# Performance work log

Measured on AMD Instinct MI355X. Metric: run time of the kernel, lower is better.

Reference implementation:

```python
import jax, jax.numpy as jnp
import numpy as np

N, E, D, S, H, L = 20000, 320000, 128, 16, 4, 64


def _ln(x, g, b):
    m = x.mean(-1, keepdims=True)
    v = jnp.mean((x - m) ** 2, -1, keepdims=True)
    return (x - m) / jnp.sqrt(v + 1e-6) * g + b


def _mlp3(x, w1, b1, g1, be1, w2, b2, g2, be2, w3, b3):
    h = jax.nn.silu(_ln(x @ w1 + b1, g1, be1))
    h = jax.nn.silu(_ln(h @ w2 + b2, g2, be2))
    return h @ w3 + b3


def _seg_softmax(a, idx, n):
    # torch_geometric.utils.softmax: per-destination-group stable softmax
    m = jax.ops.segment_max(a, idx, num_segments=n)
    m = jnp.where(jnp.isfinite(m), m, 0.0)
    e = jnp.exp(a - m[idx])
    s = jax.ops.segment_sum(e, idx, num_segments=n)
    return e / (s[idx] + 1e-16)


def setup_inputs() -> dict:
    key = jax.random.key(0)
    ks = jax.random.split(key, 32)
    rn = lambda k, sh, sc=1.0: jax.random.normal(k, sh, dtype=jnp.float32) * sc
    li = lambda k, fi, fo: rn(k, (fi, fo), 1.0 / np.sqrt(fi))
    z = lambda n_: jnp.zeros((n_,), jnp.float32)
    o = lambda n_: jnp.ones((n_,), jnp.float32)
    inp = {
        'node_in': rn(ks[0], (N, D)),
        'node_embed': rn(ks[1], (N, D)),
        'edge_sh': rn(ks[2], (E, S)),
        'edge_length_embedding': rn(ks[3], (E, L)),
        'edge_src': jax.random.randint(ks[4], (E,), 0, N, dtype=jnp.int32),
        'edge_dst': jax.random.randint(ks[5], (E,), 0, N, dtype=jnp.int32),
        'batch': jnp.zeros((N,), jnp.int32),
        'pre_lin_w': li(ks[6], 2 * D + L, D),
        'tp2_w1': li(ks[7], L, 64), 'tp2_b1': z(64),
        'tp2_w2': li(ks[8], 64, H * S), 'tp2_b2': z(H * S),
        'a_w1': li(ks[9], L, 64), 'a_b1': z(64), 'a_g1': o(64), 'a_be1': z(64),
        'a_w2': li(ks[10], 64, 64), 'a_b2': z(64), 'a_g2': o(64), 'a_be2': z(64),
        'a_w3': li(ks[11], 64, H), 'a_b3': z(H),
        'lin_w': li(ks[12], D * H, D),
        'lin_edge_w': li(ks[13], D * H, 64),
        's_w1': li(ks[14], 64, 64), 's_b1': z(64), 's_g1': o(64), 's_be1': z(64),
        's_w2': li(ks[15], 64, 64), 's_b2': z(64), 's_g2': o(64), 's_be2': z(64),
        's_w3': li(ks[16], 64, 32), 's_b3': z(32),
    }
    return inp


def reference(node_in, node_embed, edge_sh, edge_length_embedding, edge_src, edge_dst, batch,
              pre_lin_w, tp2_w1, tp2_b1, tp2_w2, tp2_b2,
              a_w1, a_b1, a_g1, a_be1, a_w2, a_b2, a_g2, a_be2, a_w3, a_b3,
              lin_w, lin_edge_w,
              s_w1, s_b1, s_g1, s_be1, s_w2, s_b2, s_g2, s_be2, s_w3, s_b3):
    e = edge_length_embedding.shape[0]
    n = node_in.shape[0]
    # gather + pre_lin
    msg = jnp.concatenate([node_in[edge_src], node_in[edge_dst], edge_length_embedding], -1) @ pre_lin_w  # [E,D]
    # EquiConv tp2: channelwise TP with radial-MLP per-edge per-(head,sh) weights
    radial = jax.nn.silu(edge_length_embedding @ tp2_w1 + tp2_b1) @ tp2_w2 + tp2_b2  # [E,H*S]
    scal = jnp.einsum('ehs,es->eh', radial.reshape(e, H, S), edge_sh)  # [E,H]
    value = msg[:, None, :] * scal[:, :, None]  # [E,H,D]
    alpha = _mlp3(edge_length_embedding, a_w1, a_b1, a_g1, a_be1, a_w2, a_b2, a_g2, a_be2, a_w3, a_b3)  # [E,H]
    edge_out = value * alpha[:, :, None]  # [E,H,D]
    edge_scalar = _mlp3(edge_out.reshape(e, -1) @ lin_edge_w,
                        s_w1, s_b1, s_g1, s_be1, s_w2, s_b2, s_g2, s_be2, s_w3, s_b3)  # [E,32]
    asm = _seg_softmax(alpha, edge_dst, n)  # [E,H]
    node_fea = jax.ops.segment_sum(value * asm[:, :, None], edge_dst, num_segments=n)  # [N,H,D]
    node_out = node_fea.reshape(n, -1) @ lin_w  # [N,D]
    return node_out, edge_scalar
```

## Files before the change

kernel.cpp:

```cpp
#include <hip/hip_runtime.h>

#define NN 20000
#define EE 320000
#define WTOT 27648
#define P3N (EE*64/8 + NN*128/8)

typedef unsigned short u16;
typedef unsigned int u32;
typedef __attribute__((ext_vector_type(8))) short bf16x8;
typedef __attribute__((ext_vector_type(8))) _Float16 f16x8;
typedef __attribute__((ext_vector_type(4))) float f32x4;

__device__ __forceinline__ float bf2f(u16 u){
  union { u32 i; float f; } v; v.i = ((u32)u) << 16; return v.f;
}
__device__ __forceinline__ u16 f2bf(float f){
  union { float f; u32 i; } v; v.f = f;
  u32 i = v.i;
  return (u16)((i + 0x7FFFu + ((i >> 16) & 1u)) >> 16);
}
__device__ __forceinline__ u16 f2h(float f){
  union { _Float16 h[2]; u32 u; } v; v.h[0] = (_Float16)f;
  return (u16)(v.u & 0xFFFF);
}
__device__ __forceinline__ float h2f(u16 u){
  union { u32 i; _Float16 h[2]; } v; v.i = u; return (float)v.h[0];
}
__device__ __forceinline__ u32 packh2(float a, float b){
  return ((u32)f2h(b) << 16) | (u32)f2h(a);
}
__device__ __forceinline__ float fsilu(float y){
  return y * __builtin_amdgcn_rcpf(1.f + __expf(-y));
}

__global__ __launch_bounds__(256) void k_prep_all(
    const float* __restrict__ elen, const float* __restrict__ node_in,
    u16* __restrict__ elen16, u16* __restrict__ node16,
    int* __restrict__ counts,
    const float* __restrict__ plw, const float* __restrict__ lew,
    const float* __restrict__ lw,
    u16* __restrict__ Bt1, u16* __restrict__ Bt2, u16* __restrict__ Bt3,
    const float* __restrict__ aw1, const float* __restrict__ aw2, const float* __restrict__ aw3,
    const float* __restrict__ rw1, const float* __restrict__ rw2,
    const float* __restrict__ sw1, const float* __restrict__ sw2, const float* __restrict__ sw3,
    u16* __restrict__ W)
{
  size_t gi = (size_t)blockIdx.x * 256 + threadIdx.x;
  if (gi < (size_t)P3N) {
    const size_t n1 = (size_t)EE * 64 / 8;
    const float* src;
    u16* dst;
    if (gi < n1) { src = elen + gi*8; dst = elen16 + gi*8; }
    else { size_t j = gi - n1; src = node_in + j*8; dst = node16 + j*8; }
    float4 a = ((const float4*)src)[0];
    float4 b = ((const float4*)src)[1];
    uint4 vh;
    vh.x = packh2(a.x, a.y); vh.y = packh2(a.z, a.w);
    vh.z = packh2(b.x, b.y); vh.w = packh2(b.z, b.w);
    *(uint4*)dst = vh;
    return;
  }
  long j = (long)gi - P3N;
  if (j < NN) { counts[j] = 0; return; }
  j -= NN;
  if (j < 128*320) {
    int n = (int)j / 320, k = (int)j % 320;
    Bt1[j] = f2h(plw[k*128 + n]);
    return;
  }
  j -= 128*320;
  if (j < 256*128) {
    int n = (int)j / 128, k = (int)j % 128;
    int h = n >> 6, c = n & 63;
    Bt2[j] = f2h(lew[(h*128 + k)*64 + c]);
    return;
  }
  j -= 256*128;
  if (j < 128*512) {
    int n = (int)j / 512, k = (int)j % 512;
    Bt3[j] = f2bf(lw[k*128 + n]);
    return;
  }
  j -= 128*512;
  if (j < WTOT) {
    float v = 0.f;
    long i = j;
    if (i < 8192)      { int n = i >> 6, k = i & 63;
                         v = (n < 64) ? aw1[k*64 + n] : rw1[k*64 + (n - 64)]; }
    else if ((i -= 8192) < 4096) { int n = i >> 6, k = i & 63; v = aw2[k*64 + n]; }
    else if ((i -= 4096) < 1024) { int n = i >> 6, k = i & 63; v = (n < 4) ? aw3[k*4 + n] : 0.f; }
    else if ((i -= 1024) < 4096) { int n = i >> 6, k = i & 63; v = rw2[k*64 + n]; }
    else if ((i -= 4096) < 4096) { int n = i >> 6, k = i & 63; v = sw1[k*64 + n]; }
    else if ((i -= 4096) < 4096) { int n = i >> 6, k = i & 63; v = sw2[k*64 + n]; }
    else               { i -= 4096; int n = i >> 6, k = i & 63; v = sw3[k*32 + n]; }
    W[j] = f2h(v);
  }
}

__global__ __launch_bounds__(256) void k_count(const int* __restrict__ edst, int* __restrict__ counts){
  int e = blockIdx.x * 256 + threadIdx.x;
  if (e < EE) atomicAdd(&counts[edst[e]], 1);
}
__global__ __launch_bounds__(1024) void k_scan(const int* __restrict__ counts,
                                               int* __restrict__ offs, int* __restrict__ cursor){
  __shared__ int part[1024];
  int t = threadIdx.x;
  int c0 = t * 20, c1 = c0 + 20; if (c1 > NN) c1 = NN; if (c0 > NN) c0 = NN;
  int s = 0;
  for (int i = c0; i < c1; ++i) s += counts[i];
  part[t] = s;
  __syncthreads();
  int acc = s;
  #pragma unroll
  for (int d = 1; d < 1024; d <<= 1) {
    int v = (t >= d) ? part[t - d] : 0;
    __syncthreads();
    acc += v;
    part[t] = acc;
    __syncthreads();
  }
  if (t == 1023) offs[NN] = acc;
  int run = acc - s;
  for (int i = c0; i < c1; ++i) { offs[i] = run; cursor[i] = run; run += counts[i]; }
}
__global__ __launch_bounds__(256) void k_fill(const int* __restrict__ edst,
                                              int* __restrict__ cursor, int* __restrict__ eids){
  int e = blockIdx.x * 256 + threadIdx.x;
  if (e < EE) { int p = atomicAdd(&cursor[edst[e]], 1); eids[p] = e; }
}
__global__ __launch_bounds__(256) void k_sort2(const int* __restrict__ offs, int* __restrict__ eids){
  int w = threadIdx.x >> 6, lane = threadIdx.x & 63;
  int n = blockIdx.x * 4 + w;
  if (n >= NN) return;
  int beg = offs[n], end = offs[n+1], deg = end - beg;
  if (deg <= 1) return;
  if (deg <= 64) {
    int v = (lane < deg) ? eids[beg + lane] : 0x7fffffff;
    int rank = 0;
    for (int j = 0; j < deg; ++j) {
      int u = __shfl(v, j);
      rank += (u < v) ? 1 : 0;
    }
    if (lane < deg) eids[beg + rank] = v;
  } else if (lane == 0) {
    for (int i = beg + 1; i < end; ++i) {
      int v = eids[i]; int j = i - 1;
      while (j >= beg && eids[j] > v) { eids[j+1] = eids[j]; --j; }
      eids[j+1] = v;
    }
  }
}

template<int NI>
__device__ __forceinline__ void gemm16_lds(const u16 (*X)[72], int wrow, int lane,
                                           const u16* __restrict__ B, f32x4 acc[2][4])
{
  const int fr = lane & 15, fc = lane >> 4;
  #pragma unroll
  for (int mi = 0; mi < 2; ++mi)
    #pragma unroll
    for (int ni = 0; ni < NI; ++ni)
      acc[mi][ni] = (f32x4){0.f, 0.f, 0.f, 0.f};
  #pragma unroll
  for (int kk = 0; kk < 2; ++kk) {
    f16x8 a0 = *(const f16x8*)&X[wrow + fr][kk*32 + fc*8];
    f16x8 a1 = *(const f16x8*)&X[wrow + 16 + fr][kk*32 + fc*8];
    #pragma unroll
    for (int ni = 0; ni < NI; ++ni) {
      f16x8 b = *(const f16x8*)(B + (size_t)(ni*16 + fr)*64 + kk*32 + fc*8);
      acc[0][ni] = __builtin_amdgcn_mfma_f32_16x16x32_f16(a0, b, acc[0][ni], 0, 0, 0);
      acc[1][ni] = __builtin_amdgcn_mfma_f32_16x16x32_f16(a1, b, acc[1][ni], 0, 0, 0);
    }
  }
}

template<int NI>
__device__ __forceinline__ void gemm16_lds1(const u16 (*X)[72], int wrow, int lane,
                                            const u16* __restrict__ B, f32x4 acc[4])
{
  const int fr = lane & 15, fc = lane >> 4;
  #pragma unroll
  for (int ni = 0; ni < NI; ++ni) acc[ni] = (f32x4){0.f, 0.f, 0.f, 0.f};
  #pragma unroll
  for (int kk = 0; kk < 2; ++kk) {
    f16x8 a = *(const f16x8*)&X[wrow + fr][kk*32 + fc*8];
    #pragma unroll
    for (int ni = 0; ni < NI; ++ni) {
      f16x8 b = *(const f16x8*)(B + (size_t)(ni*16 + fr)*64 + kk*32 + fc*8);
      acc[ni] = __builtin_amdgcn_mfma_f32_16x16x32_f16(a, b, acc[ni], 0, 0, 0);
    }
  }
}

__device__ __forceinline__ void gemm16_glb8(const u16* __restrict__ X, int row0, int lane,
                                            const u16* __restrict__ B, f32x4 acc[2][8])
{
  const int fr = lane & 15, fc = lane >> 4;
  #pragma unroll
  for (int mi = 0; mi < 2; ++mi)
    #pragma unroll
    for (int ni = 0; ni < 8; ++ni)
      acc[mi][ni] = (f32x4){0.f, 0.f, 0.f, 0.f};
  #pragma unroll
  for (int kk = 0; kk < 2; ++kk) {
    f16x8 a0 = *(const f16x8*)(X + (size_t)(row0 + fr)*64 + kk*32 + fc*8);
    f16x8 a1 = *(const f16x8*)(X + (size_t)(row0 + 16 + fr)*64 + kk*32 + fc*8);
    #pragma unroll
    for (int ni = 0; ni < 8; ++ni) {
      f16x8 b = *(const f16x8*)(B + (size_t)(ni*16 + fr)*64 + kk*32 + fc*8);
      acc[0][ni] = __builtin_amdgcn_mfma_f32_16x16x32_f16(a0, b, acc[0][ni], 0, 0, 0);
      acc[1][ni] = __builtin_amdgcn_mfma_f32_16x16x32_f16(a1, b, acc[1][ni], 0, 0, 0);
    }
  }
}

template<bool LN>
__device__ __forceinline__ void act_store16(f32x4 acc[2][4],
    const float* __restrict__ b, const float* __restrict__ g, const float* __restrict__ be,
    u16 (*H)[72], int wrow, int lane)
{
  const int fr = lane & 15, fc = lane >> 4;
  float bv[4], gv[4], bev[4];
  #pragma unroll
  for (int ni = 0; ni < 4; ++ni) {
    bv[ni] = b[ni*16 + fr];
    if (LN) { gv[ni] = g[ni*16 + fr]; bev[ni] = be[ni*16 + fr]; }
  }
  #pragma unroll
  for (int mi = 0; mi < 2; ++mi)
    #pragma unroll
    for (int j = 0; j < 4; ++j) {
      int r = wrow + mi*16 + fc*4 + j;
      float x[4];
      #pragma unroll
      for (int ni = 0; ni < 4; ++ni) x[ni] = acc[mi][ni][j] + bv[ni];
      if (LN) {
        float s  = x[0] + x[1] + x[2] + x[3];
        float s2 = x[0]*x[0] + x[1]*x[1] + x[2]*x[2] + x[3]*x[3];
        #pragma unroll
        for (int off = 1; off < 16; off <<= 1) {
          s  += __shfl_xor(s,  off);
          s2 += __shfl_xor(s2, off);
        }
        float mu  = s * (1.f/64.f);
        float var = s2 * (1.f/64.f) - mu*mu;
        float rs  = rsqrtf(var + 1e-6f);
        #pragma unroll
        for (int ni = 0; ni < 4; ++ni) x[ni] = (x[ni] - mu)*rs*gv[ni] + bev[ni];
      }
      #pragma unroll
      for (int ni = 0; ni < 4; ++ni)
        H[r][ni*16 + fr] = f2h(fsilu(x[ni]));
    }
}

template<bool LN>
__device__ __forceinline__ void act_store16_1(f32x4 acc[4],
    const float* __restrict__ b, const float* __restrict__ g, const float* __restrict__ be,
    u16 (*H)[72], int wrow, int lane)
{
  const int fr = lane & 15, fc = lane >> 4;
  float bv[4], gv[4], bev[4];
  #pragma unroll
  for (int ni = 0; ni < 4; ++ni) {
    bv[ni] = b[ni*16 + fr];
    if (LN) { gv[ni] = g[ni*16 + fr]; bev[ni] = be[ni*16 + fr]; }
  }
  #pragma unroll
  for (int j = 0; j < 4; ++j) {
    int r = wrow + fc*4 + j;
    float x[4];
    #pragma unroll
    for (int ni = 0; ni < 4; ++ni) x[ni] = acc[ni][j] + bv[ni];
    if (LN) {
      float s  = x[0] + x[1] + x[2] + x[3];
      float s2 = x[0]*x[0] + x[1]*x[1] + x[2]*x[2] + x[3]*x[3];
      #pragma unroll
      for (int off = 1; off < 16; off <<= 1) {
        s  += __shfl_xor(s,  off);
        s2 += __shfl_xor(s2, off);
      }
      float mu  = s * (1.f/64.f);
      float var = s2 * (1.f/64.f) - mu*mu;
      float rs  = rsqrtf(var + 1e-6f);
      #pragma unroll
      for (int ni = 0; ni < 4; ++ni) x[ni] = (x[ni] - mu)*rs*gv[ni] + bev[ni];
    }
    #pragma unroll
    for (int ni = 0; ni < 4; ++ni)
      H[r][ni*16 + fr] = f2h(fsilu(x[ni]));
  }
}

union ESmem {
  struct { u16 Ha[128][72]; u16 Hr[128][72]; } m;
  struct { u16 Bs[2][128][40]; } g;
};
__global__ __launch_bounds__(256, 4) void k_edge1(
  const u16* __restrict__ elen16, const float* __restrict__ esh,
  const u16* __restrict__ Wm,
  const float* __restrict__ ab1, const float* __restrict__ ag1, const float* __restrict__ abe1,
  const float* __restrict__ ab2, const float* __restrict__ ag2, const float* __restrict__ abe2,
  const float* __restrict__ ab3,
  const float* __restrict__ tb1, const float* __restrict__ tb2,
  float* __restrict__ alpha_g, float* __restrict__ scal_g, float* __restrict__ cbuf_g,
  const u16* __restrict__ node16,
  const int* __restrict__ esrc, const int* __restrict__ edst,
  const u16* __restrict__ Bt1, u16* __restrict__ msgb)
{
  __shared__ ESmem u;
  __shared__ float aS[128][4];
  const u16* Wc1 = Wm;
  const u16* Wa2 = Wm + 8192;
  const u16* Wa3 = Wm + 12288;
  const u16* Wr2 = Wm + 13312;
  const int tid = threadIdx.x;
  const int wave = tid >> 6, lane = tid & 63;
  const int fr = lane & 15, fc = lane >> 4;
  const int wrow = wave * 32;
  const int e0 = blockIdx.x * 128;
  {
    {
      f32x4 acc8[2][8];
      gemm16_glb8(elen16, e0 + wrow, lane, Wc1, acc8);
      float bva[4], gva[4], beva[4], bvr[4];
      #pragma unroll
      for (int ni = 0; ni < 4; ++ni) {
        bva[ni] = ab1[ni*16 + fr]; gva[ni] = ag1[ni*16 + fr]; beva[ni] = abe1[ni*16 + fr];
        bvr[ni] = tb1[ni*16 + fr];
      }
      #pragma unroll
      for (int mi = 0; mi < 2; ++mi)
        #pragma unroll
        for (int j = 0; j < 4; ++j) {
          int r = wrow + mi*16 + fc*4 + j;
          float xa[4], xr[4];
          #pragma unroll
          for (int ni = 0; ni < 4; ++ni) {
            xa[ni] = acc8[mi][ni][j] + bva[ni];
            xr[ni] = acc8[mi][ni+4][j] + bvr[ni];
          }
          float s  = xa[0] + xa[1] + xa[2] + xa[3];
          float s2 = xa[0]*xa[0] + xa[1]*xa[1] + xa[2]*xa[2] + xa[3]*xa[3];
          #pragma unroll
          for (int off = 1; off < 16; off <<= 1) {
            s  += __shfl_xor(s,  off);
            s2 += __shfl_xor(s2, off);
          }
          float mu  = s * (1.f/64.f);
          float var = s2 * (1.f/64.f) - mu*mu;
          float rs  = rsqrtf(var + 1e-6f);
          #pragma unroll
          for (int ni = 0; ni < 4; ++ni) {
            float y = (xa[ni] - mu)*rs*gva[ni] + beva[ni];
            u.m.Ha[r][ni*16 + fr] = f2h(fsilu(y));
            u.m.Hr[r][ni*16 + fr] = f2h(fsilu(xr[ni]));
          }
        }
    }
    f32x4 acc[2][4];
    gemm16_lds<4>(u.m.Ha, wrow, lane, Wa2, acc);
    act_store16<true>(acc, ab2, ag2, abe2, u.m.Ha, wrow, lane);
    gemm16_lds<1>(u.m.Ha, wrow, lane, Wa3, acc);
    {
      float bv = (fr < 4) ? ab3[fr] : 0.f;
      #pragma unroll
      for (int mi = 0; mi < 2; ++mi)
        #pragma unroll
        for (int j = 0; j < 4; ++j) {
          int r = wrow + mi*16 + fc*4 + j;
          float v = acc[mi][0][j] + bv;
          if (fr < 4) {
            alpha_g[(size_t)(e0 + r)*4 + fr] = v;
            aS[r][fr] = v;
          }
        }
    }
    gemm16_lds<4>(u.m.Hr, wrow, lane, Wr2, acc);
    {
      float bv[4];
      #pragma unroll
      for (int ni = 0; ni < 4; ++ni) bv[ni] = tb2[ni*16 + fr];
      #pragma unroll
      for (int mi = 0; mi < 2; ++mi)
        #pragma unroll
        for (int j = 0; j < 4; ++j) {
          int r = wrow + mi*16 + fc*4 + j;
          float shv = esh[(size_t)(e0 + r)*16 + fr];
          float sc[4];
          #pragma unroll
          for (int ni = 0; ni < 4; ++ni) {
            float t = (acc[mi][ni][j] + bv[ni]) * shv;
            #pragma unroll
            for (int off = 1; off < 16; off <<= 1) t += __shfl_xor(t, off);
            sc[ni] = t;
          }
          if (fr == 0) {
            float4 sv; sv.x = sc[0]; sv.y = sc[1]; sv.z = sc[2]; sv.w = sc[3];
            *(float4*)(scal_g + (size_t)(e0 + r)*4) = sv;
            float4 cv;
            cv.x = sc[0]*aS[r][0]; cv.y = sc[1]*aS[r][1];
            cv.z = sc[2]*aS[r][2]; cv.w = sc[3]*aS[r][3];
            *(float4*)(cbuf_g + (size_t)(e0 + r)*4) = cv;
          }
        }
    }
  }
  __syncthreads();
  {
    const int r0 = e0 + wrow + fr;
    const int r1 = r0 + 16;
    const int s0 = esrc[r0], d0 = edst[r0];
    const int s1 = esrc[r1], d1 = edst[r1];
    const int sr = tid >> 1, sh = tid & 1;
    const u16* bstg = Bt1 + (size_t)sr*320 + sh*16;
    {
      const uint4* bp = (const uint4*)(bstg);
      *(uint4*)&u.g.Bs[0][sr][sh*16]     = bp[0];
      *(uint4*)&u.g.Bs[0][sr][sh*16 + 8] = bp[1];
    }
    f32x4 acc[2][8];
    #pragma unroll
    for (int mi = 0; mi < 2; ++mi)
      #pragma unroll
      for (int ni = 0; ni < 8; ++ni)
        acc[mi][ni] = (f32x4){0.f, 0.f, 0.f, 0.f};
    __syncthreads();
    #pragma unroll
    for (int k0i = 0; k0i < 10; ++k0i) {
      const int buf = k0i & 1;
      if (k0i + 1 < 10) {
        const uint4* bp = (const uint4*)(bstg + (k0i + 1)*32);
        *(uint4*)&u.g.Bs[buf^1][sr][sh*16]     = bp[0];
        *(uint4*)&u.g.Bs[buf^1][sr][sh*16 + 8] = bp[1];
      }
      const int k0 = k0i * 32;
      const u16 *ap0, *ap1;
      if (k0 < 128)      { ap0 = node16 + (size_t)s0*128 + k0;
                           ap1 = node16 + (size_t)s1*128 + k0; }
      else if (k0 < 256) { ap0 = node16 + (size_t)d0*128 + (k0 - 128);
                           ap1 = node16 + (size_t)d1*128 + (k0 - 128); }
      else               { ap0 = elen16 + (size_t)r0*64 + (k0 - 256);
                           ap1 = elen16 + (size_t)r1*64 + (k0 - 256); }
      f16x8 a0 = *(const f16x8*)(ap0 + fc*8);
      f16x8 a1 = *(const f16x8*)(ap1 + fc*8);
      #pragma unroll
      for (int ni = 0; ni < 8; ++ni) {
        f16x8 b = *(const f16x8*)&u.g.Bs[buf][ni*16 + fr][fc*8];
        acc[0][ni] = __builtin_amdgcn_mfma_f32_16x16x32_f16(a0, b, acc[0][ni], 0, 0, 0);
        acc[1][ni] = __builtin_amdgcn_mfma_f32_16x16x32_f16(a1, b, acc[1][ni], 0, 0, 0);
      }
      __syncthreads();
    }
    #pragma unroll
    for (int mi = 0; mi < 2; ++mi)
      #pragma unroll
      for (int j = 0; j < 4; ++j) {
        int row = wrow + mi*16 + fc*4 + j;
        size_t base = (size_t)(e0 + row)*128 + fr;
        #pragma unroll
        for (int ni = 0; ni < 8; ++ni)
          msgb[base + ni*16] = f2h(acc[mi][ni][j]);
      }
  }
}

__global__ __launch_bounds__(256, 4) void g2s(
    const u16* __restrict__ msgb, const u16* __restrict__ Bt2,
    const float* __restrict__ cbuf, const u16* __restrict__ Wm,
    const float* __restrict__ b1, const float* __restrict__ g1, const float* __restrict__ be1,
    const float* __restrict__ b2, const float* __restrict__ g2, const float* __restrict__ be2,
    const float* __restrict__ b3,
    float* __restrict__ oute)
{
  __shared__ u16 Bs[256][40];
  __shared__ u16 X[64][72];
  __shared__ float cS[64][4];
  const u16* Ws1 = Wm + 17408;
  const u16* Ws2 = Wm + 21504;
  const u16* Ws3 = Wm + 25600;
  const int tid = threadIdx.x, wave = tid >> 6, lane = tid & 63;
  const int e0 = blockIdx.x * 64;
  const int fr = lane & 15, fc = lane >> 4;
  const int wrow = wave * 16;
  cS[tid >> 2][tid & 3] = cbuf[(size_t)e0*4 + tid];
  f16x8 a[4];
  {
    const u16* arow = msgb + (size_t)(e0 + wrow + fr)*128 + fc*8;
    #pragma unroll
    for (int k0i = 0; k0i < 4; ++k0i) a[k0i] = *(const f16x8*)(arow + k0i*32);
  }
  f32x4 acc[16];
  #pragma unroll
  for (int ni = 0; ni < 16; ++ni) acc[ni] = (f32x4){0.f, 0.f, 0.f, 0.f};
  const u16* bsrc = Bt2 + (size_t)tid*128;
  #pragma unroll
  for (int k0i = 0; k0i < 4; ++k0i) {
    {
      const uint4* bp = (const uint4*)(bsrc + k0i*32);
      *(uint4*)&Bs[tid][0]  = bp[0];
      *(uint4*)&Bs[tid][8]  = bp[1];
      *(uint4*)&Bs[tid][16] = bp[2];
      *(uint4*)&Bs[tid][24] = bp[3];
    }
    __syncthreads();
    #pragma unroll
    for (int ni = 0; ni < 16; ++ni) {
      f16x8 b = *(const f16x8*)&Bs[ni*16 + fr][fc*8];
      acc[ni] = __builtin_amdgcn_mfma_f32_16x16x32_f16(a[k0i], b, acc[ni], 0, 0, 0);
    }
    __syncthreads();
  }
  #pragma unroll
  for (int j = 0; j < 4; ++j) {
    int r = wrow + fc*4 + j;
    float c0 = cS[r][0], c1 = cS[r][1], c2 = cS[r][2], c3 = cS[r][3];
    #pragma unroll
    for (int m = 0; m < 4; ++m) {
      float y = c0*acc[m][j] + c1*acc[4+m][j] + c2*acc[8+m][j] + c3*acc[12+m][j];
      X[r][m*16 + fr] = f2h(y);
    }
  }
  f32x4 sa[4];
  gemm16_lds1<4>(X, wrow, lane, Ws1, sa);
  act_store16_1<true>(sa, b1, g1, be1, X, wrow, lane);
  gemm16_lds1<4>(X, wrow, lane, Ws2, sa);
  act_store16_1<true>(sa, b2, g2, be2, X, wrow, lane);
  gemm16_lds1<2>(X, wrow, lane, Ws3, sa);
  {
    float bv0 = b3[fr], bv1 = b3[16 + fr];
    #pragma unroll
    for (int j = 0; j < 4; ++j) {
      int r = wrow + fc*4 + j;
      oute[(size_t)(e0 + r)*32 + fr]      = sa[0][j] + bv0;
      oute[(size_t)(e0 + r)*32 + 16 + fr] = sa[1][j] + bv1;
    }
  }
}

__global__ __launch_bounds__(256) void k_node(
  const int* __restrict__ offs, const int* __restrict__ eids,
  const float* __restrict__ alpha, const float* __restrict__ scal,
  const u16* __restrict__ msgb, u16* __restrict__ nfb)
{
  const int w = threadIdx.x >> 6, lane = threadIdx.x & 63;
  const int n = blockIdx.x * 4 + w;
  const int beg = offs[n], end = offs[n+1];
  float m0=-3e38f, m1=-3e38f, m2=-3e38f, m3=-3e38f;
  for (int i = beg + lane; i < end; i += 64) {
    int eid = eids[i];
    float4 a = *(const float4*)(alpha + (size_t)eid*4);
    m0 = fmaxf(m0, a.x); m1 = fmaxf(m1, a.y);
    m2 = fmaxf(m2, a.z); m3 = fmaxf(m3, a.w);
  }
  #pragma unroll
  for (int off = 1; off < 64; off <<= 1) {
    m0 = fmaxf(m0, __shfl_xor(m0, off));
    m1 = fmaxf(m1, __shfl_xor(m1, off));
    m2 = fmaxf(m2, __shfl_xor(m2, off));
    m3 = fmaxf(m3, __shfl_xor(m3, off));
  }
  float se0=0.f, se1=0.f, se2=0.f, se3=0.f;
  float f00=0.f, f01=0.f, f10=0.f, f11=0.f, f20=0.f, f21=0.f, f30=0.f, f31=0.f;
  for (int i = beg; i < end; ++i) {
    int eid = eids[i];
    float4 a = *(const float4*)(alpha + (size_t)eid*4);
    float4 s = *(const float4*)(scal + (size_t)eid*4);
    float e0 = __expf(a.x - m0), e1 = __expf(a.y - m1);
    float e2 = __expf(a.z - m2), e3 = __expf(a.w - m3);
    se0 += e0; se1 += e1; se2 += e2; se3 += e3;
    float w0 = e0*s.x, w1 = e1*s.y, w2 = e2*s.z, w3 = e3*s.w;
    float v0 = h2f(msgb[(size_t)eid*128 + lane]);
    float v1 = h2f(msgb[(size_t)eid*128 + 64 + lane]);
    f00 = fmaf(w0, v0, f00); f01 = fmaf(w0, v1, f01);
    f10 = fmaf(w1, v0, f10); f11 = fmaf(w1, v1, f11);
    f20 = fmaf(w2, v0, f20); f21 = fmaf(w2, v1, f21);
    f30 = fmaf(w3, v0, f30); f31 = fmaf(w3, v1, f31);
  }
  float i0 = 1.f/(se0 + 1e-16f), i1 = 1.f/(se1 + 1e-16f);
  float i2 = 1.f/(se2 + 1e-16f), i3 = 1.f/(se3 + 1e-16f);
  size_t b = (size_t)n * 512;
  nfb[b + 0*128 + lane]      = f2bf(f00*i0);
  nfb[b + 0*128 + 64 + lane] = f2bf(f01*i0);
  nfb[b + 1*128 + lane]      = f2bf(f10*i1);
  nfb[b + 1*128 + 64 + lane] = f2bf(f11*i1);
  nfb[b + 2*128 + lane]      = f2bf(f20*i2);
  nfb[b + 2*128 + 64 + lane] = f2bf(f21*i2);
  nfb[b + 3*128 + lane]      = f2bf(f30*i3);
  nfb[b + 3*128 + 64 + lane] = f2bf(f31*i3);
}

__global__ __launch_bounds__(256) void g10_out(
    const u16* __restrict__ nfb, const u16* __restrict__ Bt3,
    float* __restrict__ out)
{
  __shared__ u16 As[128][40];
  __shared__ u16 Bs[128][40];
  const int tid = threadIdx.x;
  const int n0 = blockIdx.x * 128;
  const int wave = tid >> 6, lane = tid & 63;
  const int wr = (wave >> 1) * 64, wc = (wave & 1) * 64;
  const int fr = lane & 15, fc = lane >> 4;
  f32x4 acc[4][4] = {};
  const int r = tid >> 1, half = tid & 1;
  const int n = n0 + r;
  for (int k0 = 0; k0 < 512; k0 += 32) {
    uint4 z; z.x=0; z.y=0; z.z=0; z.w=0;
    uint4 v0 = z, v1 = z;
    if (n < NN) {
      const uint4* apv = (const uint4*)(nfb + (size_t)n*512 + k0 + half*16);
      v0 = apv[0]; v1 = apv[1];
    }
    *(uint4*)&As[r][half*16]     = v0;
    *(uint4*)&As[r][half*16 + 8] = v1;
    const uint4* bp = (const uint4*)(Bt3 + (size_t)r*512 + k0 + half*16);
    *(uint4*)&Bs[r][half*16]     = bp[0];
    *(uint4*)&Bs[r][half*16 + 8] = bp[1];
    __syncthreads();
    bf16x8 a[4], b[4];
    #pragma unroll
    for (int mi = 0; mi < 4; ++mi) a[mi] = *(const bf16x8*)&As[wr + mi*16 + fr][fc*8];
    #pragma unroll
    for (int ni = 0; ni < 4; ++ni) b[ni] = *(const bf16x8*)&Bs[wc + ni*16 + fr][fc*8];
    #pragma unroll
    for (int mi = 0; mi < 4; ++mi)
      #pragma unroll
      for (int ni = 0; ni < 4; ++ni)
        acc[mi][ni] = __builtin_amdgcn_mfma_f32_16x16x32_bf16(a[mi], b[ni], acc[mi][ni], 0, 0, 0);
    __syncthreads();
  }
  #pragma unroll
  for (int mi = 0; mi < 4; ++mi)
    #pragma unroll
    for (int j = 0; j < 4; ++j) {
      int rowg = n0 + wr + mi*16 + fc*4 + j;
      if (rowg < NN) {
        size_t base = (size_t)rowg*128 + wc + fr;
        #pragma unroll
        for (int ni = 0; ni < 4; ++ni)
          out[base + ni*16] = acc[mi][ni][j];
      }
    }
}

extern "C" void kernel_launch(void* const* d_in, const int* in_sizes, int n_in,
                              void* d_out, int out_size, void* d_ws, size_t ws_size,
                              hipStream_t stream)
{
  const float* node_in    = (const float*)d_in[0];
  const float* edge_sh    = (const float*)d_in[2];
  const float* elen       = (const float*)d_in[3];
  const int*   esrc       = (const int*)d_in[4];
  const int*   edst       = (const int*)d_in[5];
  const float* pre_lin_w  = (const float*)d_in[7];
  const float* tp2_w1     = (const float*)d_in[8];
  const float* tp2_b1     = (const float*)d_in[9];
  const float* tp2_w2     = (const float*)d_in[10];
  const float* tp2_b2     = (const float*)d_in[11];
  const float* a_w1  = (const float*)d_in[12];
  const float* a_b1  = (const float*)d_in[13];
  const float* a_g1  = (const float*)d_in[14];
  const float* a_be1 = (const float*)d_in[15];
  const float* a_w2  = (const float*)d_in[16];
  const float* a_b2  = (const float*)d_in[17];
  const float* a_g2  = (const float*)d_in[18];
  const float* a_be2 = (const float*)d_in[19];
  const float* a_w3  = (const float*)d_in[20];
  const float* a_b3  = (const float*)d_in[21];
  const float* lin_w      = (const float*)d_in[22];
  const float* lin_edge_w = (const float*)d_in[23];
  const float* s_w1  = (const float*)d_in[24];
  const float* s_b1  = (const float*)d_in[25];
  const float* s_g1  = (const float*)d_in[26];
  const float* s_be1 = (const float*)d_in[27];
  const float* s_w2  = (const float*)d_in[28];
  const float* s_b2  = (const float*)d_in[29];
  const float* s_g2  = (const float*)d_in[30];
  const float* s_be2 = (const float*)d_in[31];
  const float* s_w3  = (const float*)d_in[32];
  const float* s_b3  = (const float*)d_in[33];

  float* out_node = (float*)d_out;
  float* out_edge = out_node + (size_t)NN * 128;

  char* ws = (char*)d_ws;
  size_t off = 0;
  auto take = [&](size_t bytes) -> char* {
    char* p = ws + off;
    off = (off + bytes + 255) & ~(size_t)255;
    return p;
  };
  u16*   msgb   = (u16*)take((size_t)EE * 128 * 2);
  u16*   elen16 = (u16*)take((size_t)EE * 64 * 2);
  u16*   node16 = (u16*)take((size_t)NN * 128 * 2);
  u16*   nfb    = (u16*)take((size_t)NN * 512 * 2);
  float* alpha  = (float*)take((size_t)EE * 4 * 4);
  float* scal   = (float*)take((size_t)EE * 4 * 4);
  float* cbuf   = (float*)take((size_t)EE * 4 * 4);
  int*   counts = (int*)take((size_t)NN * 4);
  int*   offs   = (int*)take((size_t)(NN + 1) * 4);
  int*   cursor = (int*)take((size_t)NN * 4);
  int*   eids   = (int*)take((size_t)EE * 4);
  u16*   Bt1    = (u16*)take((size_t)128 * 320 * 2);
  u16*   Bt2    = (u16*)take((size_t)256 * 128 * 2);
  u16*   Bt3    = (u16*)take((size_t)128 * 512 * 2);
  u16*   Wmlp   = (u16*)take((size_t)WTOT * 2);

  const long prep_total = (long)P3N + NN + 128*320 + 256*128 + 128*512 + WTOT;
  k_prep_all<<<(int)((prep_total + 255)/256), 256, 0, stream>>>(
      elen, node_in, elen16, node16, counts,
      pre_lin_w, lin_edge_w, lin_w, Bt1, Bt2, Bt3,
      a_w1, a_w2, a_w3, tp2_w1, tp2_w2, s_w1, s_w2, s_w3, Wmlp);
  k_count<<<EE/256, 256, 0, stream>>>(edst, counts);
  k_scan<<<1, 1024, 0, stream>>>(counts, offs, cursor);
  k_fill<<<EE/256, 256, 0, stream>>>(edst, cursor, eids);
  k_sort2<<<NN/4, 256, 0, stream>>>(offs, eids);
  k_edge1<<<EE/128, 256, 0, stream>>>(elen16, edge_sh, Wmlp,
                                      a_b1, a_g1, a_be1, a_b2, a_g2, a_be2, a_b3,
                                      tp2_b1, tp2_b2, alpha, scal, cbuf,
                                      node16, esrc, edst, Bt1, msgb);
  g2s<<<EE/64, 256, 0, stream>>>(msgb, Bt2, cbuf, Wmlp,
                                 s_b1, s_g1, s_be1, s_b2, s_g2, s_be2, s_b3, out_edge);
  k_node<<<NN/4, 256, 0, stream>>>(offs, eids, alpha, scal, msgb, nfb);
  g10_out<<<(NN + 127)/128, 256, 0, stream>>>(nfb, Bt3, out_node);
}
```

Baseline: 401.7 us.

## Precompute exp(alpha) per edge, drop segment-max pass, shrink LDS row padding

```diff
diff --git a/kernel.cpp b/kernel.cpp
--- a/kernel.cpp
+++ b/kernel.cpp
@@ -152,7 +152,7 @@
 }
 
 template<int NI>
-__device__ __forceinline__ void gemm16_lds(const u16 (*X)[72], int wrow, int lane,
+__device__ __forceinline__ void gemm16_lds(const u16 (*X)[68], int wrow, int lane,
                                            const u16* __restrict__ B, f32x4 acc[2][4])
 {
   const int fr = lane & 15, fc = lane >> 4;
@@ -175,7 +175,7 @@
 }
 
 template<int NI>
-__device__ __forceinline__ void gemm16_lds1(const u16 (*X)[72], int wrow, int lane,
+__device__ __forceinline__ void gemm16_lds1(const u16 (*X)[68], int wrow, int lane,
                                             const u16* __restrict__ B, f32x4 acc[4])
 {
   const int fr = lane & 15, fc = lane >> 4;
@@ -217,7 +217,7 @@
 template<bool LN>
 __device__ __forceinline__ void act_store16(f32x4 acc[2][4],
     const float* __restrict__ b, const float* __restrict__ g, const float* __restrict__ be,
-    u16 (*H)[72], int wrow, int lane)
+    u16 (*H)[68], int wrow, int lane)
 {
   const int fr = lane & 15, fc = lane >> 4;
   float bv[4], gv[4], bev[4];
@@ -257,7 +257,7 @@
 template<bool LN>
 __device__ __forceinline__ void act_store16_1(f32x4 acc[4],
     const float* __restrict__ b, const float* __restrict__ g, const float* __restrict__ be,
-    u16 (*H)[72], int wrow, int lane)
+    u16 (*H)[68], int wrow, int lane)
 {
   const int fr = lane & 15, fc = lane >> 4;
   float bv[4], gv[4], bev[4];
@@ -293,8 +293,8 @@
 }
 
 union ESmem {
-  struct { u16 Ha[128][72]; u16 Hr[128][72]; } m;
-  struct { u16 Bs[2][128][40]; } g;
+  struct { u16 Ha[128][68]; u16 Hr[128][68]; } m;
+  struct { u16 Bs[2][128][36]; } g;
 };
 __global__ __launch_bounds__(256, 4) void k_edge1(
   const u16* __restrict__ elen16, const float* __restrict__ esh,
@@ -303,7 +303,7 @@
   const float* __restrict__ ab2, const float* __restrict__ ag2, const float* __restrict__ abe2,
   const float* __restrict__ ab3,
   const float* __restrict__ tb1, const float* __restrict__ tb2,
-  float* __restrict__ alpha_g, float* __restrict__ scal_g, float* __restrict__ cbuf_g,
+  float* __restrict__ ealpha_g, float* __restrict__ scal_g, float* __restrict__ cbuf_g,
   const u16* __restrict__ node16,
   const int* __restrict__ esrc, const int* __restrict__ edst,
   const u16* __restrict__ Bt1, u16* __restrict__ msgb)
@@ -371,7 +371,7 @@
           int r = wrow + mi*16 + fc*4 + j;
           float v = acc[mi][0][j] + bv;
           if (fr < 4) {
-            alpha_g[(size_t)(e0 + r)*4 + fr] = v;
+            ealpha_g[(size_t)(e0 + r)*4 + fr] = __expf(v);
             aS[r][fr] = v;
           }
         }
@@ -473,8 +473,8 @@
     const float* __restrict__ b3,
     float* __restrict__ oute)
 {
-  __shared__ u16 Bs[256][40];
-  __shared__ u16 X[64][72];
+  __shared__ u16 Bs[256][36];
+  __shared__ u16 X[64][68];
   __shared__ float cS[64][4];
   const u16* Ws1 = Wm + 17408;
   const u16* Ws2 = Wm + 21504;
@@ -540,36 +540,20 @@
 
 __global__ __launch_bounds__(256) void k_node(
   const int* __restrict__ offs, const int* __restrict__ eids,
-  const float* __restrict__ alpha, const float* __restrict__ scal,
+  const float* __restrict__ ealpha, const float* __restrict__ scal,
   const u16* __restrict__ msgb, u16* __restrict__ nfb)
 {
   const int w = threadIdx.x >> 6, lane = threadIdx.x & 63;
   const int n = blockIdx.x * 4 + w;
   const int beg = offs[n], end = offs[n+1];
-  float m0=-3e38f, m1=-3e38f, m2=-3e38f, m3=-3e38f;
-  for (int i = beg + lane; i < end; i += 64) {
-    int eid = eids[i];
-    float4 a = *(const float4*)(alpha + (size_t)eid*4);
-    m0 = fmaxf(m0, a.x); m1 = fmaxf(m1, a.y);
-    m2 = fmaxf(m2, a.z); m3 = fmaxf(m3, a.w);
-  }
-  #pragma unroll
-  for (int off = 1; off < 64; off <<= 1) {
-    m0 = fmaxf(m0, __shfl_xor(m0, off));
-    m1 = fmaxf(m1, __shfl_xor(m1, off));
-    m2 = fmaxf(m2, __shfl_xor(m2, off));
-    m3 = fmaxf(m3, __shfl_xor(m3, off));
-  }
   float se0=0.f, se1=0.f, se2=0.f, se3=0.f;
   float f00=0.f, f01=0.f, f10=0.f, f11=0.f, f20=0.f, f21=0.f, f30=0.f, f31=0.f;
   for (int i = beg; i < end; ++i) {
     int eid = eids[i];
-    float4 a = *(const float4*)(alpha + (size_t)eid*4);
+    float4 a = *(const float4*)(ealpha + (size_t)eid*4);
     float4 s = *(const float4*)(scal + (size_t)eid*4);
-    float e0 = __expf(a.x - m0), e1 = __expf(a.y - m1);
-    float e2 = __expf(a.z - m2), e3 = __expf(a.w - m3);
-    se0 += e0; se1 += e1; se2 += e2; se3 += e3;
-    float w0 = e0*s.x, w1 = e1*s.y, w2 = e2*s.z, w3 = e3*s.w;
+    se0 += a.x; se1 += a.y; se2 += a.z; se3 += a.w;
+    float w0 = a.x*s.x, w1 = a.y*s.y, w2 = a.z*s.z, w3 = a.w*s.w;
     float v0 = h2f(msgb[(size_t)eid*128 + lane]);
     float v1 = h2f(msgb[(size_t)eid*128 + 64 + lane]);
     f00 = fmaf(w0, v0, f00); f01 = fmaf(w0, v1, f01);
@@ -594,8 +578,8 @@
     const u16* __restrict__ nfb, const u16* __restrict__ Bt3,
     float* __restrict__ out)
 {
-  __shared__ u16 As[128][40];
-  __shared__ u16 Bs[128][40];
+  __shared__ u16 As[128][36];
+  __shared__ u16 Bs[128][36];
   const int tid = threadIdx.x;
   const int n0 = blockIdx.x * 128;
   const int wave = tid >> 6, lane = tid & 63;
@@ -694,7 +678,7 @@
   u16*   elen16 = (u16*)take((size_t)EE * 64 * 2);
   u16*   node16 = (u16*)take((size_t)NN * 128 * 2);
   u16*   nfb    = (u16*)take((size_t)NN * 512 * 2);
-  float* alpha  = (float*)take((size_t)EE * 4 * 4);
+  float* ealpha = (float*)take((size_t)EE * 4 * 4);
   float* scal   = (float*)take((size_t)EE * 4 * 4);
   float* cbuf   = (float*)take((size_t)EE * 4 * 4);
   int*   counts = (int*)take((size_t)NN * 4);
@@ -717,10 +701,10 @@
   k_sort2<<<NN/4, 256, 0, stream>>>(offs, eids);
   k_edge1<<<EE/128, 256, 0, stream>>>(elen16, edge_sh, Wmlp,
                                       a_b1, a_g1, a_be1, a_b2, a_g2, a_be2, a_b3,
-                                      tp2_b1, tp2_b2, alpha, scal, cbuf,
+                                      tp2_b1, tp2_b2, ealpha, scal, cbuf,
                                       node16, esrc, edst, Bt1, msgb);
   g2s<<<EE/64, 256, 0, stream>>>(msgb, Bt2, cbuf, Wmlp,
                                  s_b1, s_g1, s_be1, s_b2, s_g2, s_be2, s_b3, out_edge);
-  k_node<<<NN/4, 256, 0, stream>>>(offs, eids, alpha, scal, msgb, nfb);
+  k_node<<<NN/4, 256, 0, stream>>>(offs, eids, ealpha, scal, msgb, nfb);
   g10_out<<<(NN + 127)/128, 256, 0, stream>>>(nfb, Bt3, out_node);
 }
```

Result: slower. 442.3 us (+10.1%).
